# Kernel optimization log

Hardware: AMD Instinct MI355X
Metric: run time of the kernel (lower is better)

The kernel has to match this reference:

```python
import jax, jax.numpy as jnp
import numpy as np

B = 1_048_576
NUM_ITERS = 10  # training-mode default; eval mode uses 1000
EPS = 1e-12
LOW, HIGH = 0.02, 0.98  # SquashedSigmoid bounds


def setup_inputs() -> dict:
    key = jax.random.key(0)
    ks = jax.random.split(key, 4)
    # margins are population masses -> keep strictly positive
    margins = jax.random.uniform(ks[0], (B, 8), dtype=jnp.float32) + 0.1

    def lin(k, i, o):
        return (jax.random.normal(k, (i, o), jnp.float32) / np.sqrt(i)).astype(jnp.float32)

    return {
        "margins": margins,
        "W1": lin(ks[1], 8, 32), "b1": jnp.zeros((32,), jnp.float32),
        "W2": lin(ks[2], 32, 16), "b2": jnp.zeros((16,), jnp.float32),
        "W3": lin(ks[3], 16, 9), "b3": jnp.zeros((9,), jnp.float32),
    }


def tau_batched(p):
    # p: (B,4) positive params -> (B,3,3) positive couples matrix.
    # 2x2 core, extended by geometric-mean row/col (user-supplied tau in repo).
    a = p.reshape(-1, 2, 2)
    col3 = jnp.sqrt(a[:, :, 0] * a[:, :, 1])          # (B,2)
    row3 = jnp.sqrt(a[:, 0, :] * a[:, 1, :])          # (B,2)
    corner = jnp.sqrt(row3[:, 0] * row3[:, 1])        # (B,)
    top = jnp.concatenate([a, col3[:, :, None]], axis=2)                 # (B,2,3)
    bot = jnp.concatenate([row3, corner[:, None]], axis=1)[:, None, :]   # (B,1,3)
    return jnp.concatenate([top, bot], axis=1)        # (B,3,3)


def sinkhorn_knopp(A, row_margins, col_margins, iters):
    # Batched Sinkhorn-Knopp: A (B,R,C), row_margins (B,R), col_margins (B,C)
    r = row_margins[:, :, None]
    c = col_margins[:, None, :]

    def body(A, _):
        A = A * (r / (A.sum(axis=2, keepdims=True) + EPS))
        A = A * (c / (A.sum(axis=1, keepdims=True) + EPS))
        return A, None

    A, _ = jax.lax.scan(body, A, None, length=iters)
    return A


def reference(margins, W1, b1, W2, b2, W3, b3):
    Bn = margins.shape[0]
    M, F = margins[:, 0:3], margins[:, 3:6]

    # MLP: Linear-ReLU-Linear-ReLU-Linear
    h = jax.nn.relu(margins @ W1 + b1)
    h = jax.nn.relu(h @ W2 + b2)
    pars = h @ W3 + b3                                   # (B,9)

    muc = tau_batched(jnp.exp(pars[:, 0:4]))             # (B,3,3)
    sqs = lambda x: LOW + (HIGH - LOW) * jax.nn.sigmoid(x)
    shm, shf = sqs(pars[:, 4:6]), sqs(pars[:, 6:8])      # (B,2) each
    V = jnp.exp(pars[:, -1])                             # (B,)

    ones = jnp.ones((Bn, 1), margins.dtype)
    shm0 = jnp.concatenate([shm, ones], axis=1)          # (B,3)
    shf0 = jnp.concatenate([shf, ones], axis=1)          # (B,3)
    mucm0, muc0f = M * shm0, F * shf0                    # matched masses (margins)
    mum0, mu0f = M * (1.0 - shm0), F * (1.0 - shf0)      # singles

    muc = sinkhorn_knopp(muc, mucm0, muc0f, NUM_ITERS)   # (B,3,3)

    top = jnp.concatenate([muc, mum0[:, :, None]], axis=2)   # (B,3,4)
    bot = jnp.concatenate(
        [mu0f[:, None, :], jnp.zeros((Bn, 1, 1), margins.dtype)], axis=2)  # (B,1,4)
    mus = jnp.concatenate([top, bot], axis=1)            # (B,4,4)
    return mus, V
```

## Files before the change

kernel.cpp:

```cpp
#include <hip/hip_runtime.h>
#include <math.h>


#define EPS_F 1e-12f
#define QLOW  0.02f
#define QSPAN 0.96f

constexpr int R = 2;

__device__ __forceinline__ float frcp(float x) { return __builtin_amdgcn_rcpf(x); }
__device__ __forceinline__ float fsig(float x) { return frcp(1.0f + __expf(-x)); }

__global__ __launch_bounds__(256) void sinkhorn_fused(
    const float* __restrict__ margins,
    const float* __restrict__ W1, const float* __restrict__ b1,
    const float* __restrict__ W2, const float* __restrict__ b2,
    const float* __restrict__ W3, const float* __restrict__ b3,
    float* __restrict__ out, int n)
{
    __shared__ __align__(16) float sW1[256];
    __shared__ __align__(16) float sW2[512];
    __shared__ __align__(16) float sW3T[144];
    __shared__ __align__(16) float sB1[32];
    __shared__ __align__(16) float sB2[16];
    __shared__ __align__(16) float sB3[12];

    {
        const int t = threadIdx.x;
        sW1[t] = W1[t];
        sW2[t] = W2[t];
        sW2[t + 256] = W2[t + 256];
        if (t < 144) { const int k = t / 9, j = t - 9 * k; sW3T[j * 16 + k] = W3[t]; }
        if (t < 32) sB1[t] = b1[t];
        if (t < 16) sB2[t] = b2[t];
        if (t < 9)  sB3[t] = b3[t];
    }
    __syncthreads();

    const float4* __restrict__ sW1v  = (const float4*)sW1;
    const float4* __restrict__ sW2v  = (const float4*)sW2;
    const float4* __restrict__ sW3Tv = (const float4*)sW3T;

    const int tid  = blockIdx.x * blockDim.x + threadIdx.x;
    const int lane = tid & 63;
    const int base = (tid >> 6) * (64 * R) + lane;

    const float4* __restrict__ m4 = (const float4*)margins;

    float m[R][8];
#pragma unroll
    for (int r = 0; r < R; ++r) {
        const int row = base + 64 * r;
        const float4 a0 = m4[row * 2 + 0];
        const float4 a1 = m4[row * 2 + 1];
        m[r][0] = a0.x; m[r][1] = a0.y; m[r][2] = a0.z; m[r][3] = a0.w;
        m[r][4] = a1.x; m[r][5] = a1.y; m[r][6] = a1.z; m[r][7] = a1.w;
    }

    float h1[R][32];
#pragma unroll
    for (int j = 0; j < 32; ++j) {
        const float bb = sB1[j];
#pragma unroll
        for (int r = 0; r < R; ++r) h1[r][j] = bb;
    }
#pragma unroll
    for (int k = 0; k < 8; ++k) {
#pragma unroll
        for (int j4 = 0; j4 < 8; ++j4) {
            const float4 w = sW1v[k * 8 + j4];
#pragma unroll
            for (int r = 0; r < R; ++r) {
                h1[r][j4*4+0] = fmaf(m[r][k], w.x, h1[r][j4*4+0]);
                h1[r][j4*4+1] = fmaf(m[r][k], w.y, h1[r][j4*4+1]);
                h1[r][j4*4+2] = fmaf(m[r][k], w.z, h1[r][j4*4+2]);
                h1[r][j4*4+3] = fmaf(m[r][k], w.w, h1[r][j4*4+3]);
            }
        }
    }
#pragma unroll
    for (int j = 0; j < 32; ++j)
#pragma unroll
        for (int r = 0; r < R; ++r) h1[r][j] = fmaxf(h1[r][j], 0.0f);

    float h2[R][16];
#pragma unroll
    for (int j = 0; j < 16; ++j) {
        const float bb = sB2[j];
#pragma unroll
        for (int r = 0; r < R; ++r) h2[r][j] = bb;
    }
#pragma unroll
    for (int k = 0; k < 32; ++k) {
#pragma unroll
        for (int j4 = 0; j4 < 4; ++j4) {
            const float4 w = sW2v[k * 4 + j4];
#pragma unroll
            for (int r = 0; r < R; ++r) {
                h2[r][j4*4+0] = fmaf(h1[r][k], w.x, h2[r][j4*4+0]);
                h2[r][j4*4+1] = fmaf(h1[r][k], w.y, h2[r][j4*4+1]);
                h2[r][j4*4+2] = fmaf(h1[r][k], w.z, h2[r][j4*4+2]);
                h2[r][j4*4+3] = fmaf(h1[r][k], w.w, h2[r][j4*4+3]);
            }
        }
    }
#pragma unroll
    for (int j = 0; j < 16; ++j)
#pragma unroll
        for (int r = 0; r < R; ++r) h2[r][j] = fmaxf(h2[r][j], 0.0f);

    float p[R][9];
#pragma unroll
    for (int j = 0; j < 9; ++j) {
#pragma unroll
        for (int r = 0; r < R; ++r) p[r][j] = sB3[j];
#pragma unroll
        for (int k4 = 0; k4 < 4; ++k4) {
            const float4 w = sW3Tv[j * 4 + k4];
#pragma unroll
            for (int r = 0; r < R; ++r) {
                p[r][j] = fmaf(h2[r][k4*4+0], w.x, p[r][j]);
                p[r][j] = fmaf(h2[r][k4*4+1], w.y, p[r][j]);
                p[r][j] = fmaf(h2[r][k4*4+2], w.z, p[r][j]);
                p[r][j] = fmaf(h2[r][k4*4+3], w.w, p[r][j]);
            }
        }
    }

    float4* __restrict__ o4 = (float4*)out;
    float* __restrict__ oV = out + (size_t)n * 16;

#pragma unroll
    for (int r = 0; r < R; ++r) {
        const int row = base + 64 * r;

        const float e0 = __expf(p[r][0]);
        const float e1 = __expf(p[r][1]);
        const float e2 = __expf(p[r][2]);
        const float e3 = __expf(p[r][3]);
        const float col0 = sqrtf(e0 * e1);
        const float col1 = sqrtf(e2 * e3);
        const float rw0  = sqrtf(e0 * e2);
        const float rw1  = sqrtf(e1 * e3);
        const float corn = sqrtf(rw0 * rw1);

        const float a00 = e0,  a01 = e1,  a02 = col0;
        const float a10 = e2,  a11 = e3,  a12 = col1;
        const float a20 = rw0, a21 = rw1, a22 = corn;

        const float s4 = QLOW + QSPAN * fsig(p[r][4]);
        const float s5 = QLOW + QSPAN * fsig(p[r][5]);
        const float s6 = QLOW + QSPAN * fsig(p[r][6]);
        const float s7 = QLOW + QSPAN * fsig(p[r][7]);

        const float M0 = m[r][0], M1 = m[r][1], M2 = m[r][2];
        const float F0 = m[r][3], F1 = m[r][4], F2 = m[r][5];

        const float rm0 = M0 * s4, rm1 = M1 * s5, rm2 = M2;
        const float cm0 = F0 * s6, cm1 = F1 * s7, cm2 = F2;
        const float um0 = M0 * (1.0f - s4);
        const float um1 = M1 * (1.0f - s5);
        const float uf0 = F0 * (1.0f - s6);
        const float uf1 = F1 * (1.0f - s7);

        float u0 = 1.0f, u1 = 1.0f, u2 = 1.0f;
        float v0 = 1.0f, v1 = 1.0f, v2 = 1.0f;
#pragma unroll
        for (int it = 0; it < 10; ++it) {
            float t0 = fmaf(a02, v2, fmaf(a01, v1, a00 * v0));
            float t1 = fmaf(a12, v2, fmaf(a11, v1, a10 * v0));
            float t2 = fmaf(a22, v2, fmaf(a21, v1, a20 * v0));
            u0 = u0 * rm0 * frcp(fmaf(u0, t0, EPS_F));
            u1 = u1 * rm1 * frcp(fmaf(u1, t1, EPS_F));
            u2 = u2 * rm2 * frcp(fmaf(u2, t2, EPS_F));
            float s0 = fmaf(a20, u2, fmaf(a10, u1, a00 * u0));
            float s1 = fmaf(a21, u2, fmaf(a11, u1, a01 * u0));
            float s2 = fmaf(a22, u2, fmaf(a12, u1, a02 * u0));
            v0 = v0 * cm0 * frcp(fmaf(v0, s0, EPS_F));
            v1 = v1 * cm1 * frcp(fmaf(v1, s1, EPS_F));
            v2 = v2 * cm2 * frcp(fmaf(v2, s2, EPS_F));
        }

        const float A0f = u0 * a00 * v0, A1f = u0 * a01 * v1, A2f = u0 * a02 * v2;
        const float A3f = u1 * a10 * v0, A4f = u1 * a11 * v1, A5f = u1 * a12 * v2;
        const float A6f = u2 * a20 * v0, A7f = u2 * a21 * v1, A8f = u2 * a22 * v2;

        o4[row * 4 + 0] = make_float4(A0f, A1f, A2f, um0);
        o4[row * 4 + 1] = make_float4(A3f, A4f, A5f, um1);
        o4[row * 4 + 2] = make_float4(A6f, A7f, A8f, 0.0f);
        o4[row * 4 + 3] = make_float4(uf0, uf1, 0.0f, 0.0f);
        oV[row] = __expf(p[r][8]);
    }
}

extern "C" void kernel_launch(void* const* d_in, const int* in_sizes, int n_in,
                              void* d_out, int out_size, void* d_ws, size_t ws_size,
                              hipStream_t stream) {
    const float* margins = (const float*)d_in[0];
    const float* W1 = (const float*)d_in[1];
    const float* b1 = (const float*)d_in[2];
    const float* W2 = (const float*)d_in[3];
    const float* b2 = (const float*)d_in[4];
    const float* W3 = (const float*)d_in[5];
    const float* b3 = (const float*)d_in[6];

    const int n = in_sizes[0] / 8;
    const int threads = n / R;
    dim3 block(256), grid(threads / 256);

    sinkhorn_fused<<<grid, block, 0, stream>>>(margins, W1, b1, W2, b2, W3, b3,
                                               (float*)d_out, n);
}
```

Measured before the change: 133.1 us.

## Use packed FMA for MLP, drop LDS weights, compute tau in log space

Removes the shared-memory staging of the MLP weights and the block barrier, reading weights straight from global memory, which is uniform across threads and likely to become scalar loads. The three dense layers now use two-wide packed FMAs, aiming at the packed fp32 FMA instruction to halve the VALU instruction count. The tau matrix is built in log2 space with exp2 instead of exp followed by sqrt, and the Sinkhorn updates use the cancelled form u = r/t without the EPS term. Dropping EPS changes behaviour only when a row or column sum is zero, and computing in the log domain changes rounding slightly.

```diff
diff --git a/kernel.cpp b/kernel.cpp
--- a/kernel.cpp
+++ b/kernel.cpp
@@ -2,14 +2,18 @@
 #include <math.h>
 
 
-#define EPS_F 1e-12f
 #define QLOW  0.02f
 #define QSPAN 0.96f
+#define L2E   1.44269504088896f
 
 constexpr int R = 2;
 
+typedef __attribute__((ext_vector_type(2))) float f32x2;
+
 __device__ __forceinline__ float frcp(float x) { return __builtin_amdgcn_rcpf(x); }
-__device__ __forceinline__ float fsig(float x) { return frcp(1.0f + __expf(-x)); }
+__device__ __forceinline__ f32x2 pfma(f32x2 a, f32x2 b, f32x2 c) {
+    return __builtin_elementwise_fma(a, b, c);
+}
 
 __global__ __launch_bounds__(256) void sinkhorn_fused(
     const float* __restrict__ margins,
@@ -18,29 +22,6 @@
     const float* __restrict__ W3, const float* __restrict__ b3,
     float* __restrict__ out, int n)
 {
-    __shared__ __align__(16) float sW1[256];
-    __shared__ __align__(16) float sW2[512];
-    __shared__ __align__(16) float sW3T[144];
-    __shared__ __align__(16) float sB1[32];
-    __shared__ __align__(16) float sB2[16];
-    __shared__ __align__(16) float sB3[12];
-
-    {
-        const int t = threadIdx.x;
-        sW1[t] = W1[t];
-        sW2[t] = W2[t];
-        sW2[t + 256] = W2[t + 256];
-        if (t < 144) { const int k = t / 9, j = t - 9 * k; sW3T[j * 16 + k] = W3[t]; }
-        if (t < 32) sB1[t] = b1[t];
-        if (t < 16) sB2[t] = b2[t];
-        if (t < 9)  sB3[t] = b3[t];
-    }
-    __syncthreads();
-
-    const float4* __restrict__ sW1v  = (const float4*)sW1;
-    const float4* __restrict__ sW2v  = (const float4*)sW2;
-    const float4* __restrict__ sW3Tv = (const float4*)sW3T;
-
     const int tid  = blockIdx.x * blockDim.x + threadIdx.x;
     const int lane = tid & 63;
     const int base = (tid >> 6) * (64 * R) + lane;
@@ -57,73 +38,94 @@
         m[r][4] = a1.x; m[r][5] = a1.y; m[r][6] = a1.z; m[r][7] = a1.w;
     }
 
-    float h1[R][32];
-#pragma unroll
-    for (int j = 0; j < 32; ++j) {
-        const float bb = sB1[j];
+    const f32x2* __restrict__ W1v = (const f32x2*)W1;
+    const f32x2* __restrict__ W2v = (const f32x2*)W2;
+    const f32x2* __restrict__ b1v = (const f32x2*)b1;
+    const f32x2* __restrict__ b2v = (const f32x2*)b2;
+
+    f32x2 h1[R][16];
+#pragma unroll
+    for (int j = 0; j < 16; ++j) {
+        const f32x2 bb = b1v[j];
 #pragma unroll
         for (int r = 0; r < R; ++r) h1[r][j] = bb;
     }
 #pragma unroll
     for (int k = 0; k < 8; ++k) {
-#pragma unroll
-        for (int j4 = 0; j4 < 8; ++j4) {
-            const float4 w = sW1v[k * 8 + j4];
-#pragma unroll
-            for (int r = 0; r < R; ++r) {
-                h1[r][j4*4+0] = fmaf(m[r][k], w.x, h1[r][j4*4+0]);
-                h1[r][j4*4+1] = fmaf(m[r][k], w.y, h1[r][j4*4+1]);
-                h1[r][j4*4+2] = fmaf(m[r][k], w.z, h1[r][j4*4+2]);
-                h1[r][j4*4+3] = fmaf(m[r][k], w.w, h1[r][j4*4+3]);
-            }
-        }
-    }
-#pragma unroll
-    for (int j = 0; j < 32; ++j)
-#pragma unroll
-        for (int r = 0; r < R; ++r) h1[r][j] = fmaxf(h1[r][j], 0.0f);
-
-    float h2[R][16];
-#pragma unroll
-    for (int j = 0; j < 16; ++j) {
-        const float bb = sB2[j];
+        f32x2 mk[R];
+#pragma unroll
+        for (int r = 0; r < R; ++r) { mk[r].x = m[r][k]; mk[r].y = m[r][k]; }
+#pragma unroll
+        for (int j = 0; j < 16; ++j) {
+            const f32x2 w = W1v[k * 16 + j];
+#pragma unroll
+            for (int r = 0; r < R; ++r) h1[r][j] = pfma(mk[r], w, h1[r][j]);
+        }
+    }
+    const f32x2 zero2 = {0.0f, 0.0f};
+#pragma unroll
+    for (int j = 0; j < 16; ++j)
+#pragma unroll
+        for (int r = 0; r < R; ++r)
+            h1[r][j] = __builtin_elementwise_max(h1[r][j], zero2);
+
+    f32x2 h2[R][8];
+#pragma unroll
+    for (int j = 0; j < 8; ++j) {
+        const f32x2 bb = b2v[j];
 #pragma unroll
         for (int r = 0; r < R; ++r) h2[r][j] = bb;
     }
 #pragma unroll
     for (int k = 0; k < 32; ++k) {
-#pragma unroll
-        for (int j4 = 0; j4 < 4; ++j4) {
-            const float4 w = sW2v[k * 4 + j4];
-#pragma unroll
-            for (int r = 0; r < R; ++r) {
-                h2[r][j4*4+0] = fmaf(h1[r][k], w.x, h2[r][j4*4+0]);
-                h2[r][j4*4+1] = fmaf(h1[r][k], w.y, h2[r][j4*4+1]);
-                h2[r][j4*4+2] = fmaf(h1[r][k], w.z, h2[r][j4*4+2]);
-                h2[r][j4*4+3] = fmaf(h1[r][k], w.w, h2[r][j4*4+3]);
-            }
-        }
-    }
-#pragma unroll
-    for (int j = 0; j < 16; ++j)
-#pragma unroll
-        for (int r = 0; r < R; ++r) h2[r][j] = fmaxf(h2[r][j], 0.0f);
-
-    float p[R][9];
-#pragma unroll
-    for (int j = 0; j < 9; ++j) {
-#pragma unroll
-        for (int r = 0; r < R; ++r) p[r][j] = sB3[j];
-#pragma unroll
-        for (int k4 = 0; k4 < 4; ++k4) {
-            const float4 w = sW3Tv[j * 4 + k4];
-#pragma unroll
-            for (int r = 0; r < R; ++r) {
-                p[r][j] = fmaf(h2[r][k4*4+0], w.x, p[r][j]);
-                p[r][j] = fmaf(h2[r][k4*4+1], w.y, p[r][j]);
-                p[r][j] = fmaf(h2[r][k4*4+2], w.z, p[r][j]);
-                p[r][j] = fmaf(h2[r][k4*4+3], w.w, p[r][j]);
-            }
+        f32x2 hk[R];
+#pragma unroll
+        for (int r = 0; r < R; ++r) {
+            const float s = (k & 1) ? h1[r][k >> 1].y : h1[r][k >> 1].x;
+            hk[r].x = s; hk[r].y = s;
+        }
+#pragma unroll
+        for (int j = 0; j < 8; ++j) {
+            const f32x2 w = W2v[k * 8 + j];
+#pragma unroll
+            for (int r = 0; r < R; ++r) h2[r][j] = pfma(hk[r], w, h2[r][j]);
+        }
+    }
+#pragma unroll
+    for (int j = 0; j < 8; ++j)
+#pragma unroll
+        for (int r = 0; r < R; ++r)
+            h2[r][j] = __builtin_elementwise_max(h2[r][j], zero2);
+
+    f32x2 p01[R], p23[R], p45[R], p67[R];
+    float p8[R];
+    {
+        const f32x2 b01 = {b3[0], b3[1]};
+        const f32x2 b23 = {b3[2], b3[3]};
+        const f32x2 b45 = {b3[4], b3[5]};
+        const f32x2 b67 = {b3[6], b3[7]};
+        const float b8  = b3[8];
+#pragma unroll
+        for (int r = 0; r < R; ++r) {
+            p01[r] = b01; p23[r] = b23; p45[r] = b45; p67[r] = b67; p8[r] = b8;
+        }
+    }
+#pragma unroll
+    for (int k = 0; k < 16; ++k) {
+        const f32x2 w01 = {W3[k * 9 + 0], W3[k * 9 + 1]};
+        const f32x2 w23 = {W3[k * 9 + 2], W3[k * 9 + 3]};
+        const f32x2 w45 = {W3[k * 9 + 4], W3[k * 9 + 5]};
+        const f32x2 w67 = {W3[k * 9 + 6], W3[k * 9 + 7]};
+        const float w8  = W3[k * 9 + 8];
+#pragma unroll
+        for (int r = 0; r < R; ++r) {
+            const float s = (k & 1) ? h2[r][k >> 1].y : h2[r][k >> 1].x;
+            f32x2 hb; hb.x = s; hb.y = s;
+            p01[r] = pfma(hb, w01, p01[r]);
+            p23[r] = pfma(hb, w23, p23[r]);
+            p45[r] = pfma(hb, w45, p45[r]);
+            p67[r] = pfma(hb, w67, p67[r]);
+            p8[r]  = fmaf(s, w8, p8[r]);
         }
     }
 
@@ -134,62 +136,56 @@
     for (int r = 0; r < R; ++r) {
         const int row = base + 64 * r;
 
-        const float e0 = __expf(p[r][0]);
-        const float e1 = __expf(p[r][1]);
-        const float e2 = __expf(p[r][2]);
-        const float e3 = __expf(p[r][3]);
-        const float col0 = sqrtf(e0 * e1);
-        const float col1 = sqrtf(e2 * e3);
-        const float rw0  = sqrtf(e0 * e2);
-        const float rw1  = sqrtf(e1 * e3);
-        const float corn = sqrtf(rw0 * rw1);
-
-        const float a00 = e0,  a01 = e1,  a02 = col0;
-        const float a10 = e2,  a11 = e3,  a12 = col1;
-        const float a20 = rw0, a21 = rw1, a22 = corn;
-
-        const float s4 = QLOW + QSPAN * fsig(p[r][4]);
-        const float s5 = QLOW + QSPAN * fsig(p[r][5]);
-        const float s6 = QLOW + QSPAN * fsig(p[r][6]);
-        const float s7 = QLOW + QSPAN * fsig(p[r][7]);
+        const float l0 = p01[r].x * L2E, l1 = p01[r].y * L2E;
+        const float l2 = p23[r].x * L2E, l3 = p23[r].y * L2E;
+
+        const float a00 = exp2f(l0), a01 = exp2f(l1);
+        const float a10 = exp2f(l2), a11 = exp2f(l3);
+        const float h01 = (l0 + l1) * 0.5f, h23 = (l2 + l3) * 0.5f;
+        const float a02 = exp2f(h01);
+        const float a12 = exp2f(h23);
+        const float a20 = exp2f((l0 + l2) * 0.5f);
+        const float a21 = exp2f((l1 + l3) * 0.5f);
+        const float a22 = exp2f((h01 + h23) * 0.5f);
+
+        const float s4 = fmaf(QSPAN, frcp(1.0f + exp2f(-L2E * p45[r].x)), QLOW);
+        const float s5 = fmaf(QSPAN, frcp(1.0f + exp2f(-L2E * p45[r].y)), QLOW);
+        const float s6 = fmaf(QSPAN, frcp(1.0f + exp2f(-L2E * p67[r].x)), QLOW);
+        const float s7 = fmaf(QSPAN, frcp(1.0f + exp2f(-L2E * p67[r].y)), QLOW);
 
         const float M0 = m[r][0], M1 = m[r][1], M2 = m[r][2];
         const float F0 = m[r][3], F1 = m[r][4], F2 = m[r][5];
 
         const float rm0 = M0 * s4, rm1 = M1 * s5, rm2 = M2;
         const float cm0 = F0 * s6, cm1 = F1 * s7, cm2 = F2;
-        const float um0 = M0 * (1.0f - s4);
-        const float um1 = M1 * (1.0f - s5);
-        const float uf0 = F0 * (1.0f - s6);
-        const float uf1 = F1 * (1.0f - s7);
-
+        const float um0 = fmaf(-s4, M0, M0);
+        const float um1 = fmaf(-s5, M1, M1);
+        const float uf0 = fmaf(-s6, F0, F0);
+        const float uf1 = fmaf(-s7, F1, F1);
+
+        float v0 = 1.0f, v1 = 1.0f, v2 = 1.0f;
         float u0 = 1.0f, u1 = 1.0f, u2 = 1.0f;
-        float v0 = 1.0f, v1 = 1.0f, v2 = 1.0f;
 #pragma unroll
         for (int it = 0; it < 10; ++it) {
-            float t0 = fmaf(a02, v2, fmaf(a01, v1, a00 * v0));
-            float t1 = fmaf(a12, v2, fmaf(a11, v1, a10 * v0));
-            float t2 = fmaf(a22, v2, fmaf(a21, v1, a20 * v0));
-            u0 = u0 * rm0 * frcp(fmaf(u0, t0, EPS_F));
-            u1 = u1 * rm1 * frcp(fmaf(u1, t1, EPS_F));
-            u2 = u2 * rm2 * frcp(fmaf(u2, t2, EPS_F));
-            float s0 = fmaf(a20, u2, fmaf(a10, u1, a00 * u0));
-            float s1 = fmaf(a21, u2, fmaf(a11, u1, a01 * u0));
-            float s2 = fmaf(a22, u2, fmaf(a12, u1, a02 * u0));
-            v0 = v0 * cm0 * frcp(fmaf(v0, s0, EPS_F));
-            v1 = v1 * cm1 * frcp(fmaf(v1, s1, EPS_F));
-            v2 = v2 * cm2 * frcp(fmaf(v2, s2, EPS_F));
-        }
-
-        const float A0f = u0 * a00 * v0, A1f = u0 * a01 * v1, A2f = u0 * a02 * v2;
-        const float A3f = u1 * a10 * v0, A4f = u1 * a11 * v1, A5f = u1 * a12 * v2;
-        const float A6f = u2 * a20 * v0, A7f = u2 * a21 * v1, A8f = u2 * a22 * v2;
-
-        o4[row * 4 + 0] = make_float4(A0f, A1f, A2f, um0);
-        o4[row * 4 + 1] = make_float4(A3f, A4f, A5f, um1);
-        o4[row * 4 + 2] = make_float4(A6f, A7f, A8f, 0.0f);
+            const float t0 = fmaf(a02, v2, fmaf(a01, v1, a00 * v0));
+            const float t1 = fmaf(a12, v2, fmaf(a11, v1, a10 * v0));
+            const float t2 = fmaf(a22, v2, fmaf(a21, v1, a20 * v0));
+            u0 = rm0 * frcp(t0);
+            u1 = rm1 * frcp(t1);
+            u2 = rm2 * frcp(t2);
+            const float q0 = fmaf(a20, u2, fmaf(a10, u1, a00 * u0));
+            const float q1 = fmaf(a21, u2, fmaf(a11, u1, a01 * u0));
+            const float q2 = fmaf(a22, u2, fmaf(a12, u1, a02 * u0));
+            v0 = cm0 * frcp(q0);
+            v1 = cm1 * frcp(q1);
+            v2 = cm2 * frcp(q2);
+        }
+
+        o4[row * 4 + 0] = make_float4(u0 * a00 * v0, u0 * a01 * v1, u0 * a02 * v2, um0);
+        o4[row * 4 + 1] = make_float4(u1 * a10 * v0, u1 * a11 * v1, u1 * a12 * v2, um1);
+        o4[row * 4 + 2] = make_float4(u2 * a20 * v0, u2 * a21 * v1, u2 * a22 * v2, 0.0f);
         o4[row * 4 + 3] = make_float4(uf0, uf1, 0.0f, 0.0f);
-        oV[row] = __expf(p[r][8]);
+        oV[row] = exp2f(p8[r] * L2E);
     }
 }
 
```

Measured after the change: 128.0 us. 1.04x faster.
